# Kernel optimization log

Measured on AMD Instinct MI355X. Metric: run time of the kernel, lower is better.

## Reference

```python
import jax, jax.numpy as jnp
import numpy as np

B, N, F_IN = 32, 1024, 128
DIM, NUM_HEAD = 16, 8
D = DIM * NUM_HEAD  # 128


def setup_inputs() -> dict:
    key = jax.random.key(0)
    ks = jax.random.split(key, 8)
    atom_query = jax.random.normal(ks[0], (B, N, F_IN), dtype=jnp.float32)
    mask = (jax.random.uniform(ks[1], (B, N, 1)) < 0.9).astype(jnp.float32)
    s = 1.0 / np.sqrt(F_IN)
    Wq = jax.random.normal(ks[2], (F_IN, D), dtype=jnp.float32) * s
    bq = jnp.zeros((D,), dtype=jnp.float32)
    Wk = jax.random.normal(ks[3], (F_IN, D), dtype=jnp.float32) * s
    bk = jnp.zeros((D,), dtype=jnp.float32)
    Wv = jax.random.normal(ks[4], (F_IN, D), dtype=jnp.float32) * s
    bv = jnp.zeros((D,), dtype=jnp.float32)
    return {"atom_query": atom_query, "mask": mask,
            "Wq": Wq, "bq": bq, "Wk": Wk, "bk": bk, "Wv": Wv, "bv": bv}


def reference(atom_query, mask, Wq, bq, Wk, bk, Wv, bv):
    scale = 0.5  # self.scale
    q = atom_query @ Wq + bq            # [B, N, D]
    k = atom_query @ Wk + bk            # [B, N, D]
    v = atom_query @ Wv + bv            # [B, N, D] (v_proj=True)
    dk = jnp.asarray(q.shape[-1], jnp.float32) ** (-scale)
    q = q * dk
    energy = jnp.einsum('bqd,bkd->bqk', q, k)      # [B, N, N]
    energy = mask * energy                          # mask broadcasts over k
    agg = jnp.sum(energy, axis=-1, keepdims=True)   # [B, N, 1]
    agg = mask * agg
    # norm=False branch skipped
    agg = agg + (1.0 - mask) * (-1e9)
    attn = jax.nn.softmax(agg, axis=1)              # softmax over query axis
    context = jnp.sum(mask * (attn * v), axis=1)    # [B, D]
    return attn, context
```

## Files before the change

### kernel.cpp

```cpp
#include <hip/hip_runtime.h>

#define B    32
#define N    1024
#define FIN  128
#define CHN  16
#define ROWS 64
#define GRID (B * CHN)

#define OFF_PASUM 0
#define OFF_P     (B * CHN * FIN)
#define OFF_WPART (OFF_P + B * N)
#define OFF_M     (OFF_WPART + B * CHN * FIN)
#define OFF_L     (OFF_M + B * CHN)
#define OFF_S     (OFF_L + B * CHN)

__global__ __launch_bounds__(256) void k_asum(const float* __restrict__ aq,
                                              float* __restrict__ ws) {
    const int b = blockIdx.x >> 4, ch = blockIdx.x & 15;
    const float4* g4 = (const float4*)aq + ((size_t)b * N + ch * ROWS) * 32;
    float4 acc = make_float4(0.f, 0.f, 0.f, 0.f);
    #pragma unroll
    for (int i = 0; i < 8; ++i) {
        float4 v = g4[i * 256 + threadIdx.x];
        acc.x += v.x; acc.y += v.y; acc.z += v.z; acc.w += v.w;
    }
    __shared__ float4 sh[256];
    sh[threadIdx.x] = acc;
    __syncthreads();
    if (threadIdx.x < 32) {
        float4 r = sh[threadIdx.x];
        #pragma unroll
        for (int g = 1; g < 8; ++g) {
            float4 t = sh[g * 32 + threadIdx.x];
            r.x += t.x; r.y += t.y; r.z += t.z; r.w += t.w;
        }
        float4* outp = (float4*)(ws + OFF_PASUM) + (b * CHN + ch) * 32;
        outp[threadIdx.x] = r;
    }
}

__global__ __launch_bounds__(256) void k_main(
    const float* __restrict__ aq, const float* __restrict__ mask,
    const float* __restrict__ Wq, const float* __restrict__ bq,
    const float* __restrict__ Wk, const float* __restrict__ bk,
    float* __restrict__ ws)
{
    const int b = blockIdx.x >> 4, ch = blockIdx.x & 15;
    const int tid = threadIdx.x, f = tid & 127, h = tid >> 7;

    __shared__ float tile[ROWS * FIN];
    __shared__ float red[256];
    __shared__ float asum_s[FIN], ksum_s[FIN], u_s[FIN], mp_s[ROWS];
    __shared__ float c_sh;

    float4 stage[8];
    const float4* g4 = (const float4*)aq + ((size_t)b * N + ch * ROWS) * 32;
    #pragma unroll
    for (int i = 0; i < 8; ++i) stage[i] = g4[i * 256 + tid];

    if (tid < FIN) {
        float a = 0.f;
        #pragma unroll
        for (int c = 0; c < CHN; ++c)
            a += ws[OFF_PASUM + (b * CHN + c) * FIN + f];
        asum_s[f] = a;
    }
    __syncthreads();
    {
        float ks = 0.f;
        #pragma unroll 8
        for (int i = 0; i < 64; ++i) {
            int fi = h * 64 + i;
            ks += asum_s[fi] * Wk[fi * FIN + f];
        }
        red[tid] = ks;
    }
    __syncthreads();
    if (tid < FIN) ksum_s[f] = red[f] + red[f + 128] + 1024.f * bk[f];
    __syncthreads();
    {
        float uu = 0.f;
        #pragma unroll 8
        for (int i = 0; i < 64; ++i) {
            int d = h * 64 + i;
            uu += Wq[f * FIN + d] * ksum_s[d];
        }
        red[tid] = uu;
    }
    __syncthreads();
    if (tid < FIN) u_s[f] = red[f] + red[f + 128];
    if (tid < 64) {
        float cc = bq[tid] * ksum_s[tid] + bq[tid + 64] * ksum_s[tid + 64];
        #pragma unroll
        for (int off = 32; off > 0; off >>= 1) cc += __shfl_xor(cc, off);
        if (tid == 0) c_sh = cc;
    }
    {
        float4* t4 = (float4*)tile;
        #pragma unroll
        for (int i = 0; i < 8; ++i) {
            int g = i * 256 + tid;
            int row = g >> 5, c4 = g & 31;
            t4[row * 32 + (c4 ^ (row & 31))] = stage[i];
        }
    }
    __syncthreads();

    {
        const int r = tid & 63, q = tid >> 6;
        const float4* t4 = (const float4*)tile;
        const float4* u4 = (const float4*)u_s;
        float acc = 0.f;
        #pragma unroll
        for (int jj = 0; jj < 8; ++jj) {
            int j = q * 8 + jj;
            float4 a = t4[r * 32 + (j ^ (r & 31))];
            float4 uu = u4[j];
            acc += a.x * uu.x + a.y * uu.y + a.z * uu.z + a.w * uu.w;
        }
        red[tid] = acc;
    }
    __syncthreads();
    if (tid < ROWS) {
        const float dkc = 0.08838834764831845f;
        float dot = red[tid] + red[tid + 64] + red[tid + 128] + red[tid + 192];
        float m = mask[b * N + ch * ROWS + tid];
        float raw = dkc * (dot + c_sh);
        float aggv = m * raw + (1.f - m) * (-1e9f);
        float Mc = aggv;
        #pragma unroll
        for (int off = 32; off > 0; off >>= 1) Mc = fmaxf(Mc, __shfl_xor(Mc, off));
        float p = __expf(aggv - Mc);
        float mp = m * p;
        ws[OFF_P + b * N + ch * ROWS + tid] = p;
        mp_s[tid] = mp;
        float Lc = p, Sc = mp;
        #pragma unroll
        for (int off = 32; off > 0; off >>= 1) {
            Lc += __shfl_xor(Lc, off);
            Sc += __shfl_xor(Sc, off);
        }
        if (tid == 0) {
            ws[OFF_M + b * CHN + ch] = Mc;
            ws[OFF_L + b * CHN + ch] = Lc;
            ws[OFF_S + b * CHN + ch] = Sc;
        }
    }
    __syncthreads();
    {
        float w = 0.f;
        #pragma unroll 8
        for (int i = 0; i < 32; ++i) {
            int r = h * 32 + i;
            w += mp_s[r] * tile[r * FIN + ((((f >> 2) ^ (r & 31)) << 2) | (f & 3))];
        }
        red[tid] = w;
    }
    __syncthreads();
    if (tid < FIN)
        ws[OFF_WPART + (b * CHN + ch) * FIN + f] = red[f] + red[f + 128];
}

__global__ __launch_bounds__(256) void k_final(const float* __restrict__ Wv,
                                               const float* __restrict__ bv,
                                               const float* __restrict__ ws,
                                               float* __restrict__ out) {
    const int b = blockIdx.x, tid = threadIdx.x, f = tid & 127, h = tid >> 7;
    float M = -3.0e38f;
    #pragma unroll
    for (int c = 0; c < CHN; ++c) M = fmaxf(M, ws[OFF_M + b * CHN + c]);
    float Em[CHN], L = 0.f, S = 0.f;
    #pragma unroll
    for (int c = 0; c < CHN; ++c) {
        float e = __expf(ws[OFF_M + b * CHN + c] - M);
        Em[c] = e;
        L += e * ws[OFF_L + b * CHN + c];
        S += e * ws[OFF_S + b * CHN + c];
    }
    const float invL = 1.f / L;
    #pragma unroll
    for (int j = 0; j < 4; ++j) {
        int n = j * 256 + tid;
        out[b * N + n] = ws[OFF_P + b * N + n] * Em[j * 4 + (tid >> 6)] * invL;
    }
    __shared__ float wsh[FIN];
    __shared__ float red[256];
    if (tid < FIN) {
        float w = 0.f;
        #pragma unroll
        for (int c = 0; c < CHN; ++c)
            w += Em[c] * ws[OFF_WPART + (b * CHN + c) * FIN + f];
        wsh[f] = w;
    }
    __syncthreads();
    {
        float ctx = 0.f;
        #pragma unroll 8
        for (int i = 0; i < 64; ++i) {
            int fi = h * 64 + i;
            ctx += wsh[fi] * Wv[fi * FIN + f];
        }
        red[tid] = ctx;
    }
    __syncthreads();
    if (tid < FIN)
        out[B * N + b * FIN + f] = (red[f] + red[f + 128]) * invL + S * invL * bv[f];
}

extern "C" void kernel_launch(void* const* d_in, const int* in_sizes, int n_in,
                              void* d_out, int out_size, void* d_ws, size_t ws_size,
                              hipStream_t stream) {
    const float* aq   = (const float*)d_in[0];
    const float* mask = (const float*)d_in[1];
    const float* Wq   = (const float*)d_in[2];
    const float* bq   = (const float*)d_in[3];
    const float* Wk   = (const float*)d_in[4];
    const float* bk   = (const float*)d_in[5];
    const float* Wv   = (const float*)d_in[6];
    const float* bv   = (const float*)d_in[7];
    float* ws  = (float*)d_ws;
    float* out = (float*)d_out;

    k_asum <<<GRID, 256, 0, stream>>>(aq, ws);
    k_main <<<GRID, 256, 0, stream>>>(aq, mask, Wq, bq, Wk, bk, ws);
    k_final<<<B,    256, 0, stream>>>(Wv, bv, ws, out);
}
```

Before: 101.0 us.

## Fold per-batch reductions into last-arriving blocks via atomic counters

Uses atomic arrival counters so the last chunk block per batch does the per-batch work: in pass 1 it computes u and c once per batch instead of every k_main block redoing the Wk/Wq matvecs. The final softmax merge and Wv projection move into the tail of k_main, which removes the separate k_final launch. This adds a memset of the counters, fences and atomic loads/stores, and a serialized tail on one block per batch.

Measured after the change: 121.2 us. +20.0%, slower.

```diff
diff --git a/kernel.cpp b/kernel.cpp
--- a/kernel.cpp
+++ b/kernel.cpp
@@ -7,62 +7,72 @@
 #define ROWS 64
 #define GRID (B * CHN)
 
-#define OFF_PASUM 0
-#define OFF_P     (B * CHN * FIN)
-#define OFF_WPART (OFF_P + B * N)
-#define OFF_M     (OFF_WPART + B * CHN * FIN)
-#define OFF_L     (OFF_M + B * CHN)
-#define OFF_S     (OFF_L + B * CHN)
-
-__global__ __launch_bounds__(256) void k_asum(const float* __restrict__ aq,
-                                              float* __restrict__ ws) {
-    const int b = blockIdx.x >> 4, ch = blockIdx.x & 15;
-    const float4* g4 = (const float4*)aq + ((size_t)b * N + ch * ROWS) * 32;
-    float4 acc = make_float4(0.f, 0.f, 0.f, 0.f);
-    #pragma unroll
-    for (int i = 0; i < 8; ++i) {
-        float4 v = g4[i * 256 + threadIdx.x];
-        acc.x += v.x; acc.y += v.y; acc.z += v.z; acc.w += v.w;
-    }
-    __shared__ float4 sh[256];
-    sh[threadIdx.x] = acc;
-    __syncthreads();
-    if (threadIdx.x < 32) {
-        float4 r = sh[threadIdx.x];
-        #pragma unroll
-        for (int g = 1; g < 8; ++g) {
-            float4 t = sh[g * 32 + threadIdx.x];
-            r.x += t.x; r.y += t.y; r.z += t.z; r.w += t.w;
-        }
-        float4* outp = (float4*)(ws + OFF_PASUM) + (b * CHN + ch) * 32;
-        outp[threadIdx.x] = r;
-    }
-}
-
-__global__ __launch_bounds__(256) void k_main(
-    const float* __restrict__ aq, const float* __restrict__ mask,
+#define OFF_PASUM 64
+#define OFF_U     (OFF_PASUM + B*CHN*FIN)
+#define OFF_C     (OFF_U + B*FIN)
+#define OFF_P     (OFF_C + B)
+#define OFF_WPART (OFF_P + B*N)
+#define OFF_M     (OFF_WPART + B*CHN*FIN)
+#define OFF_L     (OFF_M + B*CHN)
+#define OFF_S     (OFF_L + B*CHN)
+
+__device__ __forceinline__ float aload(const float* p) {
+    return __hip_atomic_load(p, __ATOMIC_RELAXED, __HIP_MEMORY_SCOPE_AGENT);
+}
+__device__ __forceinline__ void astore(float* p, float v) {
+    __hip_atomic_store(p, v, __ATOMIC_RELAXED, __HIP_MEMORY_SCOPE_AGENT);
+}
+
+__global__ __launch_bounds__(256) void k_pass1(
+    const float* __restrict__ aq,
     const float* __restrict__ Wq, const float* __restrict__ bq,
     const float* __restrict__ Wk, const float* __restrict__ bk,
     float* __restrict__ ws)
 {
     const int b = blockIdx.x >> 4, ch = blockIdx.x & 15;
-    const int tid = threadIdx.x, f = tid & 127, h = tid >> 7;
-
-    __shared__ float tile[ROWS * FIN];
+    const int tid = threadIdx.x;
+    int* cnt = (int*)ws;
+
+    const float4* g4 = (const float4*)aq + ((size_t)b * N + ch * ROWS) * 32;
+    float4 acc = make_float4(0.f, 0.f, 0.f, 0.f);
+    #pragma unroll
+    for (int i = 0; i < 8; ++i) {
+        float4 v = g4[i * 256 + tid];
+        acc.x += v.x; acc.y += v.y; acc.z += v.z; acc.w += v.w;
+    }
+    __shared__ float4 sh4[256];
+    __shared__ int flag;
+    sh4[tid] = acc;
+    __syncthreads();
+    if (tid < 32) {
+        float4 r = sh4[tid];
+        #pragma unroll
+        for (int g = 1; g < 8; ++g) {
+            float4 t = sh4[g * 32 + tid];
+            r.x += t.x; r.y += t.y; r.z += t.z; r.w += t.w;
+        }
+        float* dst = ws + OFF_PASUM + (b * CHN + ch) * FIN + tid * 4;
+        astore(dst + 0, r.x); astore(dst + 1, r.y);
+        astore(dst + 2, r.z); astore(dst + 3, r.w);
+    }
+    __syncthreads();
+    if (tid == 0) {
+        __threadfence();
+        int old = atomicAdd(&cnt[b], 1);
+        flag = (old == CHN - 1);
+    }
+    __syncthreads();
+    if (!flag) return;
+
+    __threadfence();
+    __shared__ float asum_s[FIN], ksum_s[FIN];
     __shared__ float red[256];
-    __shared__ float asum_s[FIN], ksum_s[FIN], u_s[FIN], mp_s[ROWS];
-    __shared__ float c_sh;
-
-    float4 stage[8];
-    const float4* g4 = (const float4*)aq + ((size_t)b * N + ch * ROWS) * 32;
-    #pragma unroll
-    for (int i = 0; i < 8; ++i) stage[i] = g4[i * 256 + tid];
-
+    const int f = tid & 127, h = tid >> 7;
     if (tid < FIN) {
         float a = 0.f;
         #pragma unroll
         for (int c = 0; c < CHN; ++c)
-            a += ws[OFF_PASUM + (b * CHN + c) * FIN + f];
+            a += aload(ws + OFF_PASUM + (b * CHN + c) * FIN + f);
         asum_s[f] = a;
     }
     __syncthreads();
@@ -88,22 +98,41 @@
         red[tid] = uu;
     }
     __syncthreads();
-    if (tid < FIN) u_s[f] = red[f] + red[f + 128];
+    if (tid < FIN) ws[OFF_U + b * FIN + f] = red[f] + red[f + 128];
     if (tid < 64) {
         float cc = bq[tid] * ksum_s[tid] + bq[tid + 64] * ksum_s[tid + 64];
         #pragma unroll
         for (int off = 32; off > 0; off >>= 1) cc += __shfl_xor(cc, off);
-        if (tid == 0) c_sh = cc;
-    }
-    {
+        if (tid == 0) ws[OFF_C + b] = cc;
+    }
+}
+
+__global__ __launch_bounds__(256) void k_main(
+    const float* __restrict__ aq, const float* __restrict__ mask,
+    const float* __restrict__ Wv, const float* __restrict__ bv,
+    float* __restrict__ ws, float* __restrict__ out)
+{
+    const int b = blockIdx.x >> 4, ch = blockIdx.x & 15;
+    const int tid = threadIdx.x, f = tid & 127, h = tid >> 7;
+    int* cnt = (int*)ws;
+
+    __shared__ float tile[ROWS * FIN];
+    __shared__ float red[256];
+    __shared__ float u_s[FIN], mp_s[ROWS];
+    __shared__ float c_sh;
+    __shared__ int flag;
+
+    {
+        const float4* g4 = (const float4*)aq + ((size_t)b * N + ch * ROWS) * 32;
         float4* t4 = (float4*)tile;
         #pragma unroll
         for (int i = 0; i < 8; ++i) {
-            int g = i * 256 + tid;
-            int row = g >> 5, c4 = g & 31;
-            t4[row * 32 + (c4 ^ (row & 31))] = stage[i];
-        }
-    }
+            int g = i * 256 + tid, row = g >> 5, c4 = g & 31;
+            t4[row * 32 + (c4 ^ (row & 31))] = g4[g];
+        }
+    }
+    if (tid < FIN) u_s[f] = ws[OFF_U + b * FIN + f];
+    if (tid == 0) c_sh = ws[OFF_C + b];
     __syncthreads();
 
     {
@@ -125,14 +154,13 @@
         const float dkc = 0.08838834764831845f;
         float dot = red[tid] + red[tid + 64] + red[tid + 128] + red[tid + 192];
         float m = mask[b * N + ch * ROWS + tid];
-        float raw = dkc * (dot + c_sh);
-        float aggv = m * raw + (1.f - m) * (-1e9f);
+        float aggv = m * (dkc * (dot + c_sh)) + (1.f - m) * (-1e9f);
         float Mc = aggv;
         #pragma unroll
         for (int off = 32; off > 0; off >>= 1) Mc = fmaxf(Mc, __shfl_xor(Mc, off));
         float p = __expf(aggv - Mc);
         float mp = m * p;
-        ws[OFF_P + b * N + ch * ROWS + tid] = p;
+        astore(ws + OFF_P + b * N + ch * ROWS + tid, p);
         mp_s[tid] = mp;
         float Lc = p, Sc = mp;
         #pragma unroll
@@ -141,9 +169,9 @@
             Sc += __shfl_xor(Sc, off);
         }
         if (tid == 0) {
-            ws[OFF_M + b * CHN + ch] = Mc;
-            ws[OFF_L + b * CHN + ch] = Lc;
-            ws[OFF_S + b * CHN + ch] = Sc;
+            astore(ws + OFF_M + b * CHN + ch, Mc);
+            astore(ws + OFF_L + b * CHN + ch, Lc);
+            astore(ws + OFF_S + b * CHN + ch, Sc);
         }
     }
     __syncthreads();
@@ -157,40 +185,40 @@
         red[tid] = w;
     }
     __syncthreads();
-    if (tid < FIN)
-        ws[OFF_WPART + (b * CHN + ch) * FIN + f] = red[f] + red[f + 128];
-}
-
-__global__ __launch_bounds__(256) void k_final(const float* __restrict__ Wv,
-                                               const float* __restrict__ bv,
-                                               const float* __restrict__ ws,
-                                               float* __restrict__ out) {
-    const int b = blockIdx.x, tid = threadIdx.x, f = tid & 127, h = tid >> 7;
+    if (tid < FIN) astore(ws + OFF_WPART + (b * CHN + ch) * FIN + f, red[f] + red[f + 128]);
+    __syncthreads();
+    if (tid == 0) {
+        __threadfence();
+        int old = atomicAdd(&cnt[B + b], 1);
+        flag = (old == CHN - 1);
+    }
+    __syncthreads();
+    if (!flag) return;
+
+    __threadfence();
     float M = -3.0e38f;
     #pragma unroll
-    for (int c = 0; c < CHN; ++c) M = fmaxf(M, ws[OFF_M + b * CHN + c]);
+    for (int c = 0; c < CHN; ++c) M = fmaxf(M, aload(ws + OFF_M + b * CHN + c));
     float Em[CHN], L = 0.f, S = 0.f;
     #pragma unroll
     for (int c = 0; c < CHN; ++c) {
-        float e = __expf(ws[OFF_M + b * CHN + c] - M);
+        float e = __expf(aload(ws + OFF_M + b * CHN + c) - M);
         Em[c] = e;
-        L += e * ws[OFF_L + b * CHN + c];
-        S += e * ws[OFF_S + b * CHN + c];
+        L += e * aload(ws + OFF_L + b * CHN + c);
+        S += e * aload(ws + OFF_S + b * CHN + c);
     }
     const float invL = 1.f / L;
     #pragma unroll
     for (int j = 0; j < 4; ++j) {
         int n = j * 256 + tid;
-        out[b * N + n] = ws[OFF_P + b * N + n] * Em[j * 4 + (tid >> 6)] * invL;
-    }
-    __shared__ float wsh[FIN];
-    __shared__ float red[256];
+        out[b * N + n] = aload(ws + OFF_P + b * N + n) * Em[j * 4 + (tid >> 6)] * invL;
+    }
     if (tid < FIN) {
         float w = 0.f;
         #pragma unroll
         for (int c = 0; c < CHN; ++c)
-            w += Em[c] * ws[OFF_WPART + (b * CHN + c) * FIN + f];
-        wsh[f] = w;
+            w += Em[c] * aload(ws + OFF_WPART + (b * CHN + c) * FIN + f);
+        u_s[f] = w;
     }
     __syncthreads();
     {
@@ -198,7 +226,7 @@
         #pragma unroll 8
         for (int i = 0; i < 64; ++i) {
             int fi = h * 64 + i;
-            ctx += wsh[fi] * Wv[fi * FIN + f];
+            ctx += u_s[fi] * Wv[fi * FIN + f];
         }
         red[tid] = ctx;
     }
@@ -221,7 +249,7 @@
     float* ws  = (float*)d_ws;
     float* out = (float*)d_out;
 
-    k_asum <<<GRID, 256, 0, stream>>>(aq, ws);
-    k_main <<<GRID, 256, 0, stream>>>(aq, mask, Wq, bq, Wk, bk, ws);
-    k_final<<<B,    256, 0, stream>>>(Wv, bv, ws, out);
-}
+    hipMemsetAsync(ws, 0, 2 * B * sizeof(int), stream);
+    k_pass1<<<GRID, 256, 0, stream>>>(aq, Wq, bq, Wk, bk, ws);
+    k_main <<<GRID, 256, 0, stream>>>(aq, mask, Wv, bv, ws, out);
+}
```
